# Kernel tuning notes

Measured on AMD Instinct MI355X. Metric: run time of the kernel, lower is better.

The kernel has to match this reference:

```python
import jax, jax.numpy as jnp
import numpy as np

EPS = 1e-8  # torch F.cosine_similarity default eps


def setup_inputs() -> dict:
    key = jax.random.key(0)
    k1, k2 = jax.random.split(key)
    xs_pad = jax.random.normal(k1, (8, 4096, 512), dtype=jnp.float32)
    spk_emb = jax.random.normal(k2, (8, 256, 512), dtype=jnp.float32)
    return {"xs_pad": xs_pad, "spk_emb": spk_emb}


def reference(xs_pad, spk_emb):
    # Faithful to F.cosine_similarity(x.unsqueeze(2), y.unsqueeze(1), dim=-1):
    #   dot(x, y) / (max(||x||, eps) * max(||y||, eps))
    # Implemented as L2-normalize then a batched GEMM -> (B, T, S), avoiding
    # the (B, T, S, D) broadcast intermediate.
    x_norm = jnp.maximum(jnp.linalg.norm(xs_pad, axis=-1, keepdims=True), EPS)
    y_norm = jnp.maximum(jnp.linalg.norm(spk_emb, axis=-1, keepdims=True), EPS)
    xn = xs_pad / x_norm          # (B, T, D)
    yn = spk_emb / y_norm         # (B, S, D)
    scores = jnp.einsum('btd,bsd->bts', xn, yn)  # (B, T, S)
    return scores
```

## Files before the change

### kernel.cpp

```cpp
#include <hip/hip_runtime.h>
#include <hip/hip_bf16.h>

#define BB 8
#define TT 4096
#define SS 256
#define DD 512

typedef __attribute__((ext_vector_type(8))) short short8;
typedef __attribute__((ext_vector_type(4))) float floatx4;
typedef __attribute__((ext_vector_type(4))) int intx4;

__device__ inline int pk2(float a, float b) {
  __hip_bfloat162 h = __float22bfloat162_rn(make_float2(a, b));
  int r;
  __builtin_memcpy(&r, &h, 4);
  return r;
}

__device__ inline short8 cvt8(float4 f0, float4 f1) {
  intx4 p;
  p[0] = pk2(f0.x, f0.y);
  p[1] = pk2(f0.z, f0.w);
  p[2] = pk2(f1.x, f1.y);
  p[3] = pk2(f1.z, f1.w);
  return __builtin_bit_cast(short8, p);
}

__global__ __launch_bounds__(256) void cos_packB_kernel(
    const float* __restrict__ spk, short* __restrict__ bp) {
  const int id = blockIdx.x;
  const int ks = id & 1;
  const int kt = (id >> 1) & 7;
  const int wn = (id >> 4) & 1;
  const int tn = (id >> 5) & 1;
  const int b = id >> 6;
  const int t = threadIdx.x;
  const int in = t >> 6;
  const int lane = t & 63;
  const int row = tn * 128 + wn * 64 + in * 16 + (lane & 15);
  const int k = kt * 64 + ks * 32 + (lane >> 4) * 8;
  const float* src = spk + ((size_t)(b * SS + row)) * DD + k;
  float4 f0 = *(const float4*)src;
  float4 f1 = *(const float4*)(src + 4);
  short8 o = cvt8(f0, f1);
  size_t frag = (size_t)((((b * 2 + tn) * 2 + wn) * 8 + kt) * 2 + ks) * 4 + in;
  *(short8*)(bp + frag * 512 + (size_t)lane * 8) = o;
}

__global__ __launch_bounds__(256) void cos_fused_kernel(
    const float* __restrict__ xs, const short* __restrict__ bp,
    float* __restrict__ out) {
  __shared__ float scX[128];
  __shared__ float scY[128];

  const int tid = threadIdx.x;
  const int wave = tid >> 6;
  const int lane = tid & 63;

  const int id = blockIdx.x;
  const int xcd = id & 7;
  const int j = id >> 3;
  const int pairIdx = xcd * 32 + (j >> 1);
  const int tn = j & 1;
  const int tm = pairIdx & 31;
  const int b = pairIdx >> 5;

  const int wm = wave >> 1;
  const int wn = wave & 1;
  const int quad = lane >> 4;
  const int l15 = lane & 15;
  const bool gramA = (wm == wn);

  const float* Arow[4];
#pragma unroll
  for (int im = 0; im < 4; im++)
    Arow[im] = xs +
               ((size_t)b * TT + tm * 128 + wm * 64 + im * 16 + l15) * DD +
               quad * 8;

  const short* Bw =
      bp + (size_t)((b * 2 + tn) * 2 + wn) * 32768 + (size_t)lane * 8;

  floatx4 acc[4][4];
#pragma unroll
  for (int i = 0; i < 4; i++)
#pragma unroll
    for (int jj = 0; jj < 4; jj++) acc[i][jj] = (floatx4){0.f, 0.f, 0.f, 0.f};
  floatx4 accG[4];
#pragma unroll
  for (int i = 0; i < 4; i++) accG[i] = (floatx4){0.f, 0.f, 0.f, 0.f};

  float4 abuf[3][8];
  short8 bbuf[3][4];

#define LOADA(S)                                                        \
  do {                                                                  \
    _Pragma("unroll") for (int im_ = 0; im_ < 4; im_++) {               \
      const float* p_ = Arow[im_] + ((S) >> 1) * 64 + ((S) & 1) * 32;   \
      abuf[(S) % 3][im_ * 2] = *(const float4*)p_;                      \
      abuf[(S) % 3][im_ * 2 + 1] = *(const float4*)(p_ + 4);            \
    }                                                                   \
  } while (0)

#define LOADB(S)                                                        \
  do {                                                                  \
    const short* q_ = Bw + ((S) >> 1) * 4096 + ((S) & 1) * 2048;        \
    _Pragma("unroll") for (int in_ = 0; in_ < 4; in_++)                 \
      bbuf[(S) % 3][in_] = *(const short8*)(q_ + in_ * 512);            \
  } while (0)

  LOADA(0);
  LOADB(0);
  LOADA(1);
  LOADB(1);

#pragma unroll
  for (int s = 0; s < 16; ++s) {
    if (s + 2 < 16) {
      LOADA(s + 2);
      LOADB(s + 2);
    }

    short8 af[4];
#pragma unroll
    for (int im = 0; im < 4; im++)
      af[im] = cvt8(abuf[s % 3][im * 2], abuf[s % 3][im * 2 + 1]);

#pragma unroll
    for (int im = 0; im < 4; im++)
#pragma unroll
      for (int in = 0; in < 4; in++)
        acc[im][in] = __builtin_amdgcn_mfma_f32_16x16x32_bf16(
            af[im], bbuf[s % 3][in], acc[im][in], 0, 0, 0);
    if (gramA) {
#pragma unroll
      for (int im = 0; im < 4; im++)
        accG[im] = __builtin_amdgcn_mfma_f32_16x16x32_bf16(
            af[im], af[im], accG[im], 0, 0, 0);
    } else {
#pragma unroll
      for (int in = 0; in < 4; in++)
        accG[in] = __builtin_amdgcn_mfma_f32_16x16x32_bf16(
            bbuf[s % 3][in], bbuf[s % 3][in], accG[in], 0, 0, 0);
    }
  }
#undef LOADA
#undef LOADB

  if (quad == (l15 >> 2)) {
#pragma unroll
    for (int i = 0; i < 4; i++) {
      float inv = 1.0f / fmaxf(sqrtf(accG[i][l15 & 3]), 1e-8f);
      if (gramA)
        scX[wm * 64 + i * 16 + l15] = inv;
      else
        scY[wn * 64 + i * 16 + l15] = inv;
    }
  }
  __syncthreads();

  float* Obase = out + ((size_t)b * TT + tm * 128) * SS + tn * 128;
#pragma unroll
  for (int im = 0; im < 4; im++) {
#pragma unroll
    for (int in = 0; in < 4; in++) {
      int col = wn * 64 + in * 16 + l15;
      float yv = scY[col];
#pragma unroll
      for (int r = 0; r < 4; r++) {
        int row = wm * 64 + im * 16 + quad * 4 + r;
        Obase[row * SS + col] = acc[im][in][r] * scX[row] * yv;
      }
    }
  }
}

extern "C" void kernel_launch(void* const* d_in, const int* in_sizes, int n_in,
                              void* d_out, int out_size, void* d_ws,
                              size_t ws_size, hipStream_t stream) {
  const float* xs = (const float*)d_in[0];
  const float* spk = (const float*)d_in[1];
  float* out = (float*)d_out;
  short* bp = (short*)d_ws;

  hipLaunchKernelGGL(cos_packB_kernel, dim3(512), dim3(256), 0, stream, spk,
                     bp);
  hipLaunchKernelGGL(cos_fused_kernel, dim3(512), dim3(256), 0, stream, xs,
                     bp, out);
}
```

Measured before the change: 127.3 us.

## Stream A tiles via global_load_lds into swizzled LDS double buffer

New measurement: 124.9 us. About the same (-1.9%).

```diff
diff --git a/kernel.cpp b/kernel.cpp
--- a/kernel.cpp
+++ b/kernel.cpp
@@ -50,8 +50,9 @@
 __global__ __launch_bounds__(256) void cos_fused_kernel(
     const float* __restrict__ xs, const short* __restrict__ bp,
     float* __restrict__ out) {
-  __shared__ float scX[128];
-  __shared__ float scY[128];
+  __shared__ float sA[16384];
+  float* scX = sA;
+  float* scY = sA + 128;
 
   const int tid = threadIdx.x;
   const int wave = tid >> 6;
@@ -71,12 +72,8 @@
   const int l15 = lane & 15;
   const bool gramA = (wm == wn);
 
-  const float* Arow[4];
-#pragma unroll
-  for (int im = 0; im < 4; im++)
-    Arow[im] = xs +
-               ((size_t)b * TT + tm * 128 + wm * 64 + im * 16 + l15) * DD +
-               quad * 8;
+  const float* Aw = xs + ((size_t)b * TT + tm * 128 + wm * 64) * DD;
+  float* ldsW = sA + wave * 4096;
 
   const short* Bw =
       bp + (size_t)((b * 2 + tn) * 2 + wn) * 32768 + (size_t)lane * 8;
@@ -90,48 +87,83 @@
 #pragma unroll
   for (int i = 0; i < 4; i++) accG[i] = (floatx4){0.f, 0.f, 0.f, 0.f};
 
-  float4 abuf[3][8];
+  int soff[8];
+#pragma unroll
+  for (int o = 0; o < 8; o++) {
+    int u = o * 64 + lane;
+    int lrow = u >> 3;
+    int kblk = (u & 7) ^ (lrow & 7);
+    soff[o] = lrow * DD + kblk * 4;
+  }
+
+#define STAGE(KT)                                                          \
+  do {                                                                     \
+    _Pragma("unroll") for (int o_ = 0; o_ < 8; o_++) {                     \
+      __builtin_amdgcn_global_load_lds(                                    \
+          (const __attribute__((address_space(1))) unsigned int*)(Aw +     \
+              soff[o_] + (KT) * 32),                                       \
+          (__attribute__((address_space(3))) unsigned int*)(ldsW +         \
+              ((KT) & 1) * 2048 + o_ * 256),                               \
+          16, 0, 0);                                                       \
+    }                                                                      \
+  } while (0)
+
+#define LOADB(KT)                                                          \
+  do {                                                                     \
+    const short* q_ = Bw + ((KT) >> 1) * 4096 + ((KT) & 1) * 2048;         \
+    _Pragma("unroll") for (int in_ = 0; in_ < 4; in_++)                    \
+      bbuf[(KT) % 3][in_] = *(const short8*)(q_ + in_ * 512);              \
+  } while (0)
+
+#define WAITVM(N) asm volatile("s_waitcnt vmcnt(" #N ")" ::: "memory")
+
   short8 bbuf[3][4];
 
-#define LOADA(S)                                                        \
-  do {                                                                  \
-    _Pragma("unroll") for (int im_ = 0; im_ < 4; im_++) {               \
-      const float* p_ = Arow[im_] + ((S) >> 1) * 64 + ((S) & 1) * 32;   \
-      abuf[(S) % 3][im_ * 2] = *(const float4*)p_;                      \
-      abuf[(S) % 3][im_ * 2 + 1] = *(const float4*)(p_ + 4);            \
-    }                                                                   \
-  } while (0)
-
-#define LOADB(S)                                                        \
-  do {                                                                  \
-    const short* q_ = Bw + ((S) >> 1) * 4096 + ((S) & 1) * 2048;        \
-    _Pragma("unroll") for (int in_ = 0; in_ < 4; in_++)                 \
-      bbuf[(S) % 3][in_] = *(const short8*)(q_ + in_ * 512);            \
-  } while (0)
-
-  LOADA(0);
   LOADB(0);
-  LOADA(1);
   LOADB(1);
-
-#pragma unroll
-  for (int s = 0; s < 16; ++s) {
-    if (s + 2 < 16) {
-      LOADA(s + 2);
-      LOADB(s + 2);
+  STAGE(0);
+  STAGE(1);
+
+#pragma unroll
+  for (int kt = 0; kt < 16; ++kt) {
+    if (kt == 0)
+      WAITVM(8);
+    else if (kt == 1)
+      WAITVM(12);
+    else if (kt == 15)
+      WAITVM(4);
+    else
+      WAITVM(16);
+    __builtin_amdgcn_sched_barrier(0);
+
+    float4 f0v[4], f1v[4];
+    const float* base = ldsW + (kt & 1) * 2048;
+#pragma unroll
+    for (int im = 0; im < 4; im++) {
+      int lrow = im * 16 + l15;
+      int s0 = (quad * 2) ^ (l15 & 7);
+      int s1 = (quad * 2 + 1) ^ (l15 & 7);
+      f0v[im] = *(const float4*)(base + lrow * 32 + s0 * 4);
+      f1v[im] = *(const float4*)(base + lrow * 32 + s1 * 4);
+    }
+    asm volatile("s_waitcnt lgkmcnt(0)" ::: "memory");
+    __builtin_amdgcn_sched_barrier(0);
+
+    if (kt + 2 < 16) {
+      STAGE(kt + 2);
+      LOADB(kt + 2);
     }
 
     short8 af[4];
 #pragma unroll
-    for (int im = 0; im < 4; im++)
-      af[im] = cvt8(abuf[s % 3][im * 2], abuf[s % 3][im * 2 + 1]);
+    for (int im = 0; im < 4; im++) af[im] = cvt8(f0v[im], f1v[im]);
 
 #pragma unroll
     for (int im = 0; im < 4; im++)
 #pragma unroll
       for (int in = 0; in < 4; in++)
         acc[im][in] = __builtin_amdgcn_mfma_f32_16x16x32_bf16(
-            af[im], bbuf[s % 3][in], acc[im][in], 0, 0, 0);
+            af[im], bbuf[kt % 3][in], acc[im][in], 0, 0, 0);
     if (gramA) {
 #pragma unroll
       for (int im = 0; im < 4; im++)
@@ -141,11 +173,14 @@
 #pragma unroll
       for (int in = 0; in < 4; in++)
         accG[in] = __builtin_amdgcn_mfma_f32_16x16x32_bf16(
-            bbuf[s % 3][in], bbuf[s % 3][in], accG[in], 0, 0, 0);
-    }
-  }
-#undef LOADA
+            bbuf[kt % 3][in], bbuf[kt % 3][in], accG[in], 0, 0, 0);
+    }
+  }
+#undef STAGE
 #undef LOADB
+#undef WAITVM
+
+  __syncthreads();
 
   if (quad == (l15 >> 2)) {
 #pragma unroll
```
